# Performance work log

Hardware: AMD Instinct MI355X
Metric: run time of the kernel (lower is better)

The kernel has to match this reference:

```python
import jax, jax.numpy as jnp
import numpy as np

B, NQ, NKV, K = 2, 1024, 2048, 64
D, H, LAT = 1024, 16, 128
HD = D // H
SCALE = 1.0 / np.sqrt(HD)


def setup_inputs() -> dict:
    key = jax.random.key(0)
    ks = jax.random.split(key, 7)
    s = lambda fan_in: 1.0 / np.sqrt(fan_in)
    return {
        "x_q": jax.random.normal(ks[0], (B, NQ, D), jnp.float32),
        "x_kv": jax.random.normal(ks[1], (B, NKV, D), jnp.float32),
        "indices": jax.random.randint(ks[2], (B, NQ, K), 0, NKV),
        "W_q": jax.random.normal(ks[3], (D, D), jnp.float32) * s(D),
        "W_kv_down": jax.random.normal(ks[4], (LAT, D), jnp.float32) * s(D),
        "W_kv_up": jax.random.normal(ks[5], (2 * D, LAT), jnp.float32) * s(LAT),
        "W_out": jax.random.normal(ks[6], (D, D), jnp.float32) * s(D),
    }


def reference(x_q, x_kv, indices, W_q, W_kv_down, W_kv_up, W_out):
    b, nq, d = x_q.shape
    # q: (B, NQ, H, HD)
    q = (x_q @ W_q.T).reshape(b, nq, H, HD)
    # latent KV cache: (B, NKV, LAT)
    c_kv = x_kv @ W_kv_down.T
    # per-query gather of selected latents: (B, NQ, K, LAT)
    c_sel = c_kv[jnp.arange(b)[:, None, None], indices]
    # up-project to k/v heads: (B, NQ, K, 2, H, HD)
    kv = (c_sel @ W_kv_up.T).reshape(b, nq, K, 2, H, HD)
    k = kv[:, :, :, 0]  # (B, NQ, K, H, HD)
    v = kv[:, :, :, 1]
    # selective attention: scores over the K selected positions
    scores = jnp.einsum("bqhd,bqkhd->bqkh", q, k) * SCALE
    attn = jax.nn.softmax(scores, axis=2)
    out = jnp.einsum("bqkh,bqkhd->bqhd", attn, v).reshape(b, nq, d)
    return out @ W_out.T
```

## Files before the change

kernel.cpp:

```cpp
#include <hip/hip_runtime.h>

#define NKVc  2048
#define SCALE 0.125f

typedef unsigned short u16;
typedef __attribute__((ext_vector_type(8))) short short8b;
typedef __attribute__((ext_vector_type(8))) unsigned short ushort8;
typedef __attribute__((ext_vector_type(4))) float f32x4;

__device__ __forceinline__ u16 f2bf(float f) {
  unsigned int u = __float_as_uint(f);
  return (u16)((u + 0x7FFFu + ((u >> 16) & 1u)) >> 16);
}

__device__ __forceinline__ void conv8(const float* __restrict__ in,
                                      u16* __restrict__ out, int j) {
  float4 f0 = ((const float4*)in)[j * 2];
  float4 f1 = ((const float4*)in)[j * 2 + 1];
  ushort4 a, b;
  a.x = f2bf(f0.x); a.y = f2bf(f0.y); a.z = f2bf(f0.z); a.w = f2bf(f0.w);
  b.x = f2bf(f1.x); b.y = f2bf(f1.y); b.z = f2bf(f1.z); b.w = f2bf(f1.w);
  ((ushort4*)out)[j * 2] = a;
  ((ushort4*)out)[j * 2 + 1] = b;
}

__global__ __launch_bounds__(256)
void megaconv(const float* __restrict__ xq, const float* __restrict__ wq,
              const float* __restrict__ xkv, const float* __restrict__ wkvd,
              const float* __restrict__ wkvu, const float* __restrict__ wout,
              u16* __restrict__ xq_bf, u16* __restrict__ wq_bf,
              u16* __restrict__ xkv_bf, u16* __restrict__ wkvd_bf,
              u16* __restrict__ wv_bf, u16* __restrict__ wout_bf,
              u16* __restrict__ wkt) {
  int i = blockIdx.x * 256 + threadIdx.x;
  if (i < 262144) { conv8(xq, xq_bf, i); return; }
  if (i < 393216) { conv8(wq, wq_bf, i - 262144); return; }
  if (i < 917504) { conv8(xkv, xkv_bf, i - 393216); return; }
  if (i < 933888) { conv8(wkvd, wkvd_bf, i - 917504); return; }
  if (i < 950272) { conv8(wkvu + 131072, wv_bf, i - 933888); return; }
  if (i < 1081344) { conv8(wout, wout_bf, i - 950272); return; }
  {
    int o = (i - 1081344) * 8;
    int hd0 = o & 63;
    int l = (o >> 6) & 127;
    int h = o >> 13;
    const float* src = wkvu + (h * 64 + hd0) * 128 + l;
    ushort8 v;
#pragma unroll
    for (int j = 0; j < 8; ++j) v[j] = f2bf(src[j * 128]);
    *(ushort8*)&wkt[o] = v;
  }
}

__device__ __forceinline__ void gemm_body(
    int bx, int by, int bz,
    const u16* __restrict__ A, int lda, long sAz,
    const u16* __restrict__ B, int ldb, long sBz,
    float* __restrict__ C, u16* __restrict__ Cb,
    int ldc, long sCz, int K, bool obf) {
  A += (size_t)bz * sAz;
  B += (size_t)bz * sBz;
  __shared__ __align__(16) u16 As[2][512 * 8];
  __shared__ __align__(16) u16 Bs[2][512 * 8];
  const int tid = threadIdx.x;
  const int w = tid >> 6, lane = tid & 63;
  const int bm = by * 64, bn = bx * 64;
  const int wr = w >> 1, wc = w & 1;

  f32x4 acc[2][2] = {};

  auto stage = [&](int buf, int t) {
#pragma unroll
    for (int sub = 0; sub < 2; ++sub) {
      int s = w * 64 + lane;
      int row = s >> 2;
      int kc = (s & 3) ^ ((row >> 1) & 3);
      int kg = t * 64 + sub * 32 + kc * 8;
      {
        const u16* g = A + (size_t)(bm + row) * lda + kg;
        __builtin_amdgcn_global_load_lds(
            (const __attribute__((address_space(1))) unsigned int*)g,
            (__attribute__((address_space(3))) unsigned int*)&As[buf][(sub * 256 + w * 64) * 8],
            16, 0, 0);
      }
      {
        const u16* g = B + (size_t)(bn + row) * ldb + kg;
        __builtin_amdgcn_global_load_lds(
            (const __attribute__((address_space(1))) unsigned int*)g,
            (__attribute__((address_space(3))) unsigned int*)&Bs[buf][(sub * 256 + w * 64) * 8],
            16, 0, 0);
      }
    }
  };

  auto compute = [&](int buf) {
#pragma unroll
    for (int sub = 0; sub < 2; ++sub) {
      short8b a[2], b[2];
#pragma unroll
      for (int m = 0; m < 2; ++m) {
        int row = wr * 32 + m * 16 + (lane & 15);
        int slot = sub * 256 + row * 4 + ((lane >> 4) ^ ((row >> 1) & 3));
        a[m] = *(const short8b*)&As[buf][slot * 8];
      }
#pragma unroll
      for (int n = 0; n < 2; ++n) {
        int col = wc * 32 + n * 16 + (lane & 15);
        int slot = sub * 256 + col * 4 + ((lane >> 4) ^ ((col >> 1) & 3));
        b[n] = *(const short8b*)&Bs[buf][slot * 8];
      }
#pragma unroll
      for (int m = 0; m < 2; ++m)
#pragma unroll
        for (int n = 0; n < 2; ++n)
          acc[m][n] = __builtin_amdgcn_mfma_f32_16x16x32_bf16(a[m], b[n], acc[m][n], 0, 0, 0);
    }
  };

  stage(0, 0);
  asm volatile("s_waitcnt vmcnt(0)" ::: "memory");
  __syncthreads();
  const int nk = K >> 6;
  for (int t = 0; t < nk; ++t) {
    int cur = t & 1;
    if (t + 1 < nk) stage(cur ^ 1, t + 1);
    compute(cur);
    asm volatile("s_waitcnt vmcnt(0)" ::: "memory");
    __syncthreads();
  }

#pragma unroll
  for (int m = 0; m < 2; ++m) {
    int row0 = bm + wr * 32 + m * 16 + (lane >> 4) * 4;
#pragma unroll
    for (int n = 0; n < 2; ++n) {
      int col = bn + wc * 32 + n * 16 + (lane & 15);
      if (obf) {
        u16* Cz = Cb + (size_t)bz * sCz;
#pragma unroll
        for (int r = 0; r < 4; ++r)
          Cz[(size_t)(row0 + r) * ldc + col] = f2bf(acc[m][n][r]);
      } else {
        float* Cz = C + (size_t)bz * sCz;
#pragma unroll
        for (int r = 0; r < 4; ++r)
          Cz[(size_t)(row0 + r) * ldc + col] = acc[m][n][r];
      }
    }
  }
}

__global__ __launch_bounds__(256)
void gemm_nt_g(const u16* __restrict__ A, int lda, long sAz,
               const u16* __restrict__ B, int ldb, long sBz,
               float* __restrict__ C, u16* __restrict__ Cb,
               int ldc, long sCz, int K, int obf) {
  gemm_body(blockIdx.x, blockIdx.y, blockIdx.z, A, lda, sAz, B, ldb, sBz,
            C, Cb, ldc, sCz, K, obf != 0);
}

__global__ __launch_bounds__(256)
void d1_qproj_ckv(const u16* __restrict__ xq_bf, const u16* __restrict__ wq_bf,
                  const u16* __restrict__ xkv_bf, const u16* __restrict__ wkvd_bf,
                  u16* __restrict__ q_bf, float* __restrict__ pbuf) {
  int b = blockIdx.x;
  if (b < 512) {
    gemm_body(b & 15, b >> 4, 0, xq_bf, 1024, 0, wq_bf, 1024, 0,
              nullptr, q_bf, 1024, 0, 1024, true);
  } else {
    int b2 = b - 512;
    gemm_body(b2 & 1, (b2 >> 1) & 63, b2 >> 7, xkv_bf, 1024, 256,
              wkvd_bf, 1024, 256, pbuf, nullptr, 128, (long)4096 * 128,
              256, false);
  }
}

__global__ __launch_bounds__(256)
void d2_qlat_reduce(const u16* __restrict__ q_bf, const u16* __restrict__ wkt,
                    u16* __restrict__ qlat_bf, const float* __restrict__ pbuf,
                    u16* __restrict__ c_kvb) {
  int b = blockIdx.x;
  if (b >= 1024) {
    int i = (b - 1024) * 256 + threadIdx.x;
    const float4* s = (const float4*)pbuf;
    float4 a = s[i], bb = s[i + 131072], c = s[i + 2 * 131072], d = s[i + 3 * 131072];
    ushort4 v;
    v.x = f2bf(a.x + bb.x + c.x + d.x); v.y = f2bf(a.y + bb.y + c.y + d.y);
    v.z = f2bf(a.z + bb.z + c.z + d.z); v.w = f2bf(a.w + bb.w + c.w + d.w);
    ((ushort4*)c_kvb)[i] = v;
    return;
  }
  int bz = b >> 6, r = b & 63;
  gemm_body(r & 1, r >> 1, bz, q_bf, 1024, 64, wkt, 64, 8192,
            nullptr, qlat_bf, 2048, 128, 64, true);
}

__global__ __launch_bounds__(256)
void attn_mfma(const u16* __restrict__ c_kvb,
               const u16* __restrict__ q_latb,
               const int* __restrict__ indices,
               u16* __restrict__ cw_bf) {
  __shared__ __align__(16) u16 qls[256 * 8];
  __shared__ __align__(16) u16 csa[1024 * 8];
  __shared__ __align__(16) u16 cst[128 * 72];
  __shared__ __align__(16) u16 pT[16 * 72];
  __shared__ __align__(16) float redmax[64];
  __shared__ __align__(16) float redsum[64];
  __shared__ __align__(16) u16 outst[2048];

  const int tid = threadIdx.x;
  const int w = tid >> 6, lane = tid & 63;
  const int bq = blockIdx.x;
  const int b = bq >> 10;

  {
    int h = tid >> 4, c = tid & 15;
    ushort8 v = *(const ushort8*)(q_latb + (size_t)bq * 2048 + tid * 8);
    *(ushort8*)&qls[(h * 16 + (c ^ h)) * 8] = v;
  }
  {
    int kidx = indices[bq * 64 + lane];
    const u16* src = c_kvb + ((size_t)b * NKVc + kidx) * 128 + w * 32;
    ushort8 v[4];
#pragma unroll
    for (int t = 0; t < 4; ++t) v[t] = *(const ushort8*)(src + t * 8);
#pragma unroll
    for (int t = 0; t < 4; ++t) {
      int c = w * 4 + t;
      *(ushort8*)&csa[(lane * 16 + (c ^ (lane & 15))) * 8] = v[t];
    }
#pragma unroll
    for (int t = 0; t < 4; ++t)
#pragma unroll
      for (int j = 0; j < 8; ++j)
        cst[(w * 32 + t * 8 + j) * 72 + lane] = v[t][j];
  }
  __syncthreads();

  f32x4 sacc = {};
#pragma unroll
  for (int kc = 0; kc < 4; ++kc) {
    int ar = w * 16 + (lane & 15);
    int ac = kc * 4 + (lane >> 4);
    short8b av = *(const short8b*)&csa[(ar * 16 + (ac ^ (ar & 15))) * 8];
    int bh = lane & 15;
    short8b bv = *(const short8b*)&qls[(bh * 16 + (ac ^ bh)) * 8];
    sacc = __builtin_amdgcn_mfma_f32_16x16x32_bf16(av, bv, sacc, 0, 0, 0);
  }
  float s0 = sacc[0] * SCALE, s1 = sacc[1] * SCALE;
  float s2 = sacc[2] * SCALE, s3 = sacc[3] * SCALE;
  float mx = fmaxf(fmaxf(s0, s1), fmaxf(s2, s3));
  mx = fmaxf(mx, __shfl_xor(mx, 16));
  mx = fmaxf(mx, __shfl_xor(mx, 32));
  if (lane < 16) redmax[w * 16 + lane] = mx;
  __syncthreads();
  const int h = lane & 15;
  float m4 = fmaxf(fmaxf(redmax[h], redmax[16 + h]),
                   fmaxf(redmax[32 + h], redmax[48 + h]));
  float p0 = __expf(s0 - m4), p1 = __expf(s1 - m4);
  float p2 = __expf(s2 - m4), p3 = __expf(s3 - m4);
  float sm = p0 + p1 + p2 + p3;
  sm += __shfl_xor(sm, 16);
  sm += __shfl_xor(sm, 32);
  if (lane < 16) redsum[w * 16 + lane] = sm;
  __syncthreads();
  float tot = redsum[h] + redsum[16 + h] + redsum[32 + h] + redsum[48 + h];
  float inv = 1.0f / tot;
  {
    ushort4 pw;
    pw.x = f2bf(p0 * inv); pw.y = f2bf(p1 * inv);
    pw.z = f2bf(p2 * inv); pw.w = f2bf(p3 * inv);
    *(ushort4*)&pT[h * 72 + w * 16 + (lane >> 4) * 4] = pw;
  }
  __syncthreads();

  f32x4 pacc0 = {}, pacc1 = {};
#pragma unroll
  for (int kc = 0; kc < 2; ++kc) {
    short8b pa = *(const short8b*)&pT[(lane & 15) * 72 + kc * 32 + (lane >> 4) * 8];
    int cch = kc * 4 + (lane >> 4);
    int n0 = w * 32 + (lane & 15);
    short8b b0 = *(const short8b*)&cst[n0 * 72 + cch * 8];
    short8b b1 = *(const short8b*)&cst[(n0 + 16) * 72 + cch * 8];
    pacc0 = __builtin_amdgcn_mfma_f32_16x16x32_bf16(pa, b0, pacc0, 0, 0, 0);
    pacc1 = __builtin_amdgcn_mfma_f32_16x16x32_bf16(pa, b1, pacc1, 0, 0, 0);
  }
#pragma unroll
  for (int r = 0; r < 4; ++r) {
    int hh = (lane >> 4) * 4 + r;
    outst[hh * 128 + w * 32 + (lane & 15)] = f2bf(pacc0[r]);
    outst[hh * 128 + w * 32 + 16 + (lane & 15)] = f2bf(pacc1[r]);
  }
  __syncthreads();
  *(ushort8*)(cw_bf + (size_t)bq * 2048 + tid * 8) = *(const ushort8*)&outst[tid * 8];
}

extern "C" void kernel_launch(void* const* d_in, const int* in_sizes, int n_in,
                              void* d_out, int out_size, void* d_ws, size_t ws_size,
                              hipStream_t stream) {
  const float* x_q    = (const float*)d_in[0];
  const float* x_kv   = (const float*)d_in[1];
  const int*   idx    = (const int*)  d_in[2];
  const float* W_q    = (const float*)d_in[3];
  const float* W_kvd  = (const float*)d_in[4];
  const float* W_kvu  = (const float*)d_in[5];
  const float* W_out  = (const float*)d_in[6];
  float* out = (float*)d_out;

  char* wsb = (char*)d_ws;
  u16* xq_bf   = (u16*)(wsb + 0);
  u16* wq_bf   = (u16*)(wsb + (4u << 20));
  u16* xkv_bf  = (u16*)(wsb + (6u << 20));
  u16* wkvd_bf = (u16*)(wsb + (14u << 20));
  u16* wkt     = (u16*)(wsb + (14u << 20) + (256u << 10));
  u16* wv_bf   = (u16*)(wsb + (14u << 20) + (512u << 10));
  u16* wout_bf = (u16*)(wsb + (14u << 20) + (768u << 10));
  u16* q_bf    = (u16*)(wsb + (17u << 20));
  u16* c_kvb   = (u16*)(wsb + (21u << 20));
  u16* qlat_bf = (u16*)(wsb + (22u << 20));
  u16* cw_bf   = (u16*)(wsb + (30u << 20));
  u16* o_bf    = (u16*)(wsb + (38u << 20));
  float* pbuf  = (float*)(wsb + (30u << 20));

  megaconv<<<dim3(4288), 256, 0, stream>>>(x_q, W_q, x_kv, W_kvd, W_kvu, W_out,
                                           xq_bf, wq_bf, xkv_bf, wkvd_bf,
                                           wv_bf, wout_bf, wkt);

  d1_qproj_ckv<<<dim3(1024), 256, 0, stream>>>(xq_bf, wq_bf, xkv_bf, wkvd_bf,
                                               q_bf, pbuf);

  d2_qlat_reduce<<<dim3(1536), 256, 0, stream>>>(q_bf, wkt, qlat_bf, pbuf, c_kvb);

  attn_mfma<<<dim3(2048), 256, 0, stream>>>(c_kvb, qlat_bf, idx, cw_bf);

  gemm_nt_g<<<dim3(1, 32, 16), 256, 0, stream>>>(
      cw_bf, 2048, 128, wv_bf, 128, 8192, nullptr, o_bf, 1024, 64, 128, 1);

  gemm_nt_g<<<dim3(16, 32, 1), 256, 0, stream>>>(
      o_bf, 1024, 0, wout_bf, 1024, 0, out, nullptr, 1024, 0, 1024, 0);
}
```

Before: 66.05 us.

## Drop split-K for c_kv projection and use deeper K tiles in later GEMMs

The c_kv down-projection no longer uses a 4-way split-K with an fp32 partial buffer and a separate reduction pass. It now runs as a single full-K GEMM that writes bf16 directly, and the reduction blocks are removed from the qlat kernel. The GEMM body is templated on the K-substep count, and the value-up and output projections use 128-wide K tiles (doubling LDS per block) to halve the number of loop iterations and barriers. The trade-off is fewer blocks with longer serial K loops for c_kv, and lower occupancy from the larger LDS footprint.

```diff
diff --git a/kernel.cpp b/kernel.cpp
--- a/kernel.cpp
+++ b/kernel.cpp
@@ -52,6 +52,7 @@
   }
 }
 
+template<int NSUB>
 __device__ __forceinline__ void gemm_body(
     int bx, int by, int bz,
     const u16* __restrict__ A, int lda, long sAz,
@@ -60,8 +61,8 @@
     int ldc, long sCz, int K, bool obf) {
   A += (size_t)bz * sAz;
   B += (size_t)bz * sBz;
-  __shared__ __align__(16) u16 As[2][512 * 8];
-  __shared__ __align__(16) u16 Bs[2][512 * 8];
+  __shared__ __align__(16) u16 As[2][NSUB * 256 * 8];
+  __shared__ __align__(16) u16 Bs[2][NSUB * 256 * 8];
   const int tid = threadIdx.x;
   const int w = tid >> 6, lane = tid & 63;
   const int bm = by * 64, bn = bx * 64;
@@ -71,11 +72,11 @@
 
   auto stage = [&](int buf, int t) {
 #pragma unroll
-    for (int sub = 0; sub < 2; ++sub) {
+    for (int sub = 0; sub < NSUB; ++sub) {
       int s = w * 64 + lane;
       int row = s >> 2;
       int kc = (s & 3) ^ ((row >> 1) & 3);
-      int kg = t * 64 + sub * 32 + kc * 8;
+      int kg = t * (NSUB * 32) + sub * 32 + kc * 8;
       {
         const u16* g = A + (size_t)(bm + row) * lda + kg;
         __builtin_amdgcn_global_load_lds(
@@ -95,7 +96,7 @@
 
   auto compute = [&](int buf) {
 #pragma unroll
-    for (int sub = 0; sub < 2; ++sub) {
+    for (int sub = 0; sub < NSUB; ++sub) {
       short8b a[2], b[2];
 #pragma unroll
       for (int m = 0; m < 2; ++m) {
@@ -120,7 +121,7 @@
   stage(0, 0);
   asm volatile("s_waitcnt vmcnt(0)" ::: "memory");
   __syncthreads();
-  const int nk = K >> 6;
+  const int nk = K / (NSUB * 32);
   for (int t = 0; t < nk; ++t) {
     int cur = t & 1;
     if (t + 1 < nk) stage(cur ^ 1, t + 1);
@@ -151,48 +152,36 @@
 }
 
 __global__ __launch_bounds__(256)
-void gemm_nt_g(const u16* __restrict__ A, int lda, long sAz,
-               const u16* __restrict__ B, int ldb, long sBz,
-               float* __restrict__ C, u16* __restrict__ Cb,
-               int ldc, long sCz, int K, int obf) {
-  gemm_body(blockIdx.x, blockIdx.y, blockIdx.z, A, lda, sAz, B, ldb, sBz,
-            C, Cb, ldc, sCz, K, obf != 0);
+void gemm_nt_g4(const u16* __restrict__ A, int lda, long sAz,
+                const u16* __restrict__ B, int ldb, long sBz,
+                float* __restrict__ C, u16* __restrict__ Cb,
+                int ldc, long sCz, int K, int obf) {
+  gemm_body<4>(blockIdx.x, blockIdx.y, blockIdx.z, A, lda, sAz, B, ldb, sBz,
+               C, Cb, ldc, sCz, K, obf != 0);
 }
 
 __global__ __launch_bounds__(256)
 void d1_qproj_ckv(const u16* __restrict__ xq_bf, const u16* __restrict__ wq_bf,
                   const u16* __restrict__ xkv_bf, const u16* __restrict__ wkvd_bf,
-                  u16* __restrict__ q_bf, float* __restrict__ pbuf) {
+                  u16* __restrict__ q_bf, u16* __restrict__ c_kvb) {
   int b = blockIdx.x;
   if (b < 512) {
-    gemm_body(b & 15, b >> 4, 0, xq_bf, 1024, 0, wq_bf, 1024, 0,
-              nullptr, q_bf, 1024, 0, 1024, true);
+    gemm_body<2>(b & 15, b >> 4, 0, xq_bf, 1024, 0, wq_bf, 1024, 0,
+                 nullptr, q_bf, 1024, 0, 1024, true);
   } else {
     int b2 = b - 512;
-    gemm_body(b2 & 1, (b2 >> 1) & 63, b2 >> 7, xkv_bf, 1024, 256,
-              wkvd_bf, 1024, 256, pbuf, nullptr, 128, (long)4096 * 128,
-              256, false);
-  }
-}
-
-__global__ __launch_bounds__(256)
-void d2_qlat_reduce(const u16* __restrict__ q_bf, const u16* __restrict__ wkt,
-                    u16* __restrict__ qlat_bf, const float* __restrict__ pbuf,
-                    u16* __restrict__ c_kvb) {
+    gemm_body<2>(b2 & 1, b2 >> 1, 0, xkv_bf, 1024, 0, wkvd_bf, 1024, 0,
+                 nullptr, c_kvb, 128, 0, 1024, true);
+  }
+}
+
+__global__ __launch_bounds__(256)
+void d2_qlat(const u16* __restrict__ q_bf, const u16* __restrict__ wkt,
+             u16* __restrict__ qlat_bf) {
   int b = blockIdx.x;
-  if (b >= 1024) {
-    int i = (b - 1024) * 256 + threadIdx.x;
-    const float4* s = (const float4*)pbuf;
-    float4 a = s[i], bb = s[i + 131072], c = s[i + 2 * 131072], d = s[i + 3 * 131072];
-    ushort4 v;
-    v.x = f2bf(a.x + bb.x + c.x + d.x); v.y = f2bf(a.y + bb.y + c.y + d.y);
-    v.z = f2bf(a.z + bb.z + c.z + d.z); v.w = f2bf(a.w + bb.w + c.w + d.w);
-    ((ushort4*)c_kvb)[i] = v;
-    return;
-  }
   int bz = b >> 6, r = b & 63;
-  gemm_body(r & 1, r >> 1, bz, q_bf, 1024, 64, wkt, 64, 8192,
-            nullptr, qlat_bf, 2048, 128, 64, true);
+  gemm_body<2>(r & 1, r >> 1, bz, q_bf, 1024, 64, wkt, 64, 8192,
+               nullptr, qlat_bf, 2048, 128, 64, true);
 }
 
 __global__ __launch_bounds__(256)
@@ -320,22 +309,21 @@
   u16* qlat_bf = (u16*)(wsb + (22u << 20));
   u16* cw_bf   = (u16*)(wsb + (30u << 20));
   u16* o_bf    = (u16*)(wsb + (38u << 20));
-  float* pbuf  = (float*)(wsb + (30u << 20));
 
   megaconv<<<dim3(4288), 256, 0, stream>>>(x_q, W_q, x_kv, W_kvd, W_kvu, W_out,
                                            xq_bf, wq_bf, xkv_bf, wkvd_bf,
                                            wv_bf, wout_bf, wkt);
 
-  d1_qproj_ckv<<<dim3(1024), 256, 0, stream>>>(xq_bf, wq_bf, xkv_bf, wkvd_bf,
-                                               q_bf, pbuf);
-
-  d2_qlat_reduce<<<dim3(1536), 256, 0, stream>>>(q_bf, wkt, qlat_bf, pbuf, c_kvb);
+  d1_qproj_ckv<<<dim3(640), 256, 0, stream>>>(xq_bf, wq_bf, xkv_bf, wkvd_bf,
+                                              q_bf, c_kvb);
+
+  d2_qlat<<<dim3(1024), 256, 0, stream>>>(q_bf, wkt, qlat_bf);
 
   attn_mfma<<<dim3(2048), 256, 0, stream>>>(c_kvb, qlat_bf, idx, cw_bf);
 
-  gemm_nt_g<<<dim3(1, 32, 16), 256, 0, stream>>>(
+  gemm_nt_g4<<<dim3(1, 32, 16), 256, 0, stream>>>(
       cw_bf, 2048, 128, wv_bf, 128, 8192, nullptr, o_bf, 1024, 64, 128, 1);
 
-  gemm_nt_g<<<dim3(16, 32, 1), 256, 0, stream>>>(
+  gemm_nt_g4<<<dim3(16, 32, 1), 256, 0, stream>>>(
       o_bf, 1024, 0, wout_bf, 1024, 0, out, nullptr, 1024, 0, 1024, 0);
 }
```

Result: faster. 63.69 us (-3.6%).
